# Optimization experiments

Measured on AMD Instinct MI355X. Metric: run time of the kernel, lower is better.

Reference implementation:

```python
import jax, jax.numpy as jnp
import numpy as np
from jax import lax

EPS = 1e-5
K = 7
G = 4


def _dwconv_bn(x, w, g, b, m, v):
    # depthwise 3x3, pad 1, then BN (eval mode with running stats)
    C = x.shape[1]
    y = lax.conv_general_dilated(x, w, (1, 1), [(1, 1), (1, 1)],
                                 feature_group_count=C,
                                 dimension_numbers=('NCHW', 'OIHW', 'NCHW'))
    scale = (g / jnp.sqrt(v + EPS))[None, :, None, None]
    return (y - m[None, :, None, None]) * scale + b[None, :, None, None]


def _proj(t, pw1, pb1, pw2, pb2):
    # 1x1 conv -> GELU(exact) -> 1x1 conv, on small spatial maps
    h = jnp.einsum('bchw,oc->bohw', t, pw1) + pb1[None, :, None, None]
    h = jax.nn.gelu(h, approximate=False)
    return jnp.einsum('bchw,oc->bohw', h, pw2) + pb2[None, :, None, None]


def setup_inputs() -> dict:
    key = jax.random.key(0)
    ks = jax.random.split(key, 17)
    B, C, H, W = 16, 256, 56, 56
    r = C // 4
    inp = {
        'x1': jax.random.normal(ks[0], (B, C, H, W), jnp.float32),
        'dw1_w': jax.random.normal(ks[1], (C, 1, 3, 3), jnp.float32) * 0.1,
        'dw1_g': jax.random.uniform(ks[2], (C,), jnp.float32, 0.5, 1.5),
        'dw1_b': jax.random.normal(ks[3], (C,), jnp.float32) * 0.1,
        'dw1_m': jax.random.normal(ks[4], (C,), jnp.float32) * 0.1,
        'dw1_v': jax.random.uniform(ks[5], (C,), jnp.float32, 0.5, 1.5),
        'dw2_w': jax.random.normal(ks[6], (C, 1, 3, 3), jnp.float32) * 0.1,
        'dw2_g': jax.random.uniform(ks[7], (C,), jnp.float32, 0.5, 1.5),
        'dw2_b': jax.random.normal(ks[8], (C,), jnp.float32) * 0.1,
        'dw2_m': jax.random.normal(ks[9], (C,), jnp.float32) * 0.1,
        'dw2_v': jax.random.uniform(ks[10], (C,), jnp.float32, 0.5, 1.5),
        'weight1': jax.random.normal(ks[11], (G, C, K, K), jnp.float32) * 0.02,
        'bias1': jax.random.normal(ks[12], (G, C), jnp.float32) * 0.02,
        'pw1': jax.random.normal(ks[13], (r, C), jnp.float32) * 0.05,
        'pb1': jax.random.normal(ks[14], (r,), jnp.float32) * 0.05,
        'pw2': jax.random.normal(ks[15], (C * G, r), jnp.float32) * 0.05,
        'pb2': jax.random.normal(ks[16], (C * G,), jnp.float32) * 0.05,
    }
    return inp


def reference(x1, dw1_w, dw1_g, dw1_b, dw1_m, dw1_v,
              dw2_w, dw2_g, dw2_b, dw2_m, dw2_v,
              weight1, bias1, pw1, pb1, pw2, pb2):
    B, C, H, W = x1.shape
    # gated fuse: relu6(dw1(x)) * dw2(x)
    a = jnp.clip(_dwconv_bn(x1, dw1_w, dw1_g, dw1_b, dw1_m, dw1_v), 0.0, 6.0)
    x_fuse = a * _dwconv_bn(x1, dw2_w, dw2_g, dw2_b, dw2_m, dw2_v)

    # adaptive avg pool to (K,K): H,W multiples of K -> uniform block means
    pooled = x_fuse.reshape(B, C, K, H // K, K, W // K).mean(axis=(3, 5))

    # dynamic kernel: proj -> softmax over groups -> weighted sum of weight1
    scale1 = _proj(pooled, pw1, pb1, pw2, pb2).reshape(B, G, C, K, K)
    scale1 = jax.nn.softmax(scale1, axis=1)
    w_dyn = jnp.sum(scale1 * weight1[None], axis=1)  # [B, C, K, K]

    # dynamic bias
    mean_x = x_fuse.mean(axis=(-2, -1), keepdims=True)  # [B, C, 1, 1]
    sb = _proj(mean_x, pw1, pb1, pw2, pb2).reshape(B, G, C)
    sb = jax.nn.softmax(sb, axis=1)
    b_dyn = jnp.sum(sb * bias1[None], axis=1)  # [B, C]

    # per-sample depthwise conv with dynamic weights
    pad = K // 2

    def per_sample(xi, wi):  # xi [C,H,W], wi [C,K,K]
        y = lax.conv_general_dilated(xi[None], wi[:, None], (1, 1),
                                     [(pad, pad), (pad, pad)],
                                     feature_group_count=C,
                                     dimension_numbers=('NCHW', 'OIHW', 'NCHW'))
        return y[0]

    out = jax.vmap(per_sample)(x_fuse, w_dyn)  # [B, C, H, W]
    return out + b_dyn[:, :, None, None]
```

## Files before the change

kernel.cpp:

```cpp
#include <hip/hip_runtime.h>
#include <math.h>

#define BATCH 16
#define CH 256
#define HW 56
#define NPIX (HW*HW)
#define PR 62
#define PS 64
#define PPLANE (PR*PS)

__device__ __forceinline__ void fuse_tile(
    const float* __restrict__ plane, int ty, int tx,
    const float w1[9], const float w2[9],
    float sc1, float be1, float sc2, float be2,
    float res[4][4])
{
    const int oy = 4 * ty;
    float y1a[4][4], y2a[4][4];
    #pragma unroll
    for (int a = 0; a < 4; a++)
        #pragma unroll
        for (int e = 0; e < 4; e++) { y1a[a][e] = 0.f; y2a[a][e] = 0.f; }

    #pragma unroll
    for (int iy = 0; iy < 6; iy++) {
        const int r    = oy - 1 + iy;
        const bool rok = (r >= 0) && (r < 56);
        const int rc   = rok ? r : 0;
        float rb[12];
        #pragma unroll
        for (int k = 0; k < 3; k++) {
            const int cx  = tx - 1 + k;
            const bool cv = (cx >= 0) && (cx < 14);
            const int cc2 = cv ? cx : 0;
            const bool ok = rok && cv;
            float4 v = *(const float4*)(plane + rc*56 + 4*cc2);
            rb[4*k+0] = ok ? v.x : 0.f;
            rb[4*k+1] = ok ? v.y : 0.f;
            rb[4*k+2] = ok ? v.z : 0.f;
            rb[4*k+3] = ok ? v.w : 0.f;
        }
        #pragma unroll
        for (int tyy = 0; tyy < 4; tyy++) {
            const int ky = iy - tyy;
            if (ky >= 0 && ky < 3) {
                #pragma unroll
                for (int e = 0; e < 4; e++)
                    #pragma unroll
                    for (int dj = 0; dj < 3; dj++) {
                        float xv = rb[3 + e + dj];
                        y1a[tyy][e] += xv * w1[ky*3+dj];
                        y2a[tyy][e] += xv * w2[ky*3+dj];
                    }
            }
        }
    }
    #pragma unroll
    for (int tyy = 0; tyy < 4; tyy++)
        #pragma unroll
        for (int e = 0; e < 4; e++) {
            float y1 = y1a[tyy][e] * sc1 + be1;
            float y2 = y2a[tyy][e] * sc2 + be2;
            float a = fminf(fmaxf(y1, 0.f), 6.f);
            res[tyy][e] = a * y2;
        }
}

__global__ __launch_bounds__(256) void k1_fuse(
    const float* __restrict__ x1,
    const float* __restrict__ dw1w, const float* __restrict__ g1, const float* __restrict__ b1,
    const float* __restrict__ m1, const float* __restrict__ v1,
    const float* __restrict__ dw2w, const float* __restrict__ g2, const float* __restrict__ b2,
    const float* __restrict__ m2, const float* __restrict__ v2,
    float* __restrict__ xf,
    float* __restrict__ pooled)
{
    const int bc = blockIdx.x;
    const int c  = bc & 255;
    const int t  = threadIdx.x;

    __shared__ float part[196];

    float w1[9], w2[9];
    #pragma unroll
    for (int k = 0; k < 9; k++) { w1[k] = dw1w[c*9+k]; w2[k] = dw2w[c*9+k]; }
    const float sc1 = g1[c] * rsqrtf(v1[c] + 1e-5f);
    const float be1 = b1[c] - m1[c] * sc1;
    const float sc2 = g2[c] * rsqrtf(v2[c] + 1e-5f);
    const float be2 = b2[c] - m2[c] * sc2;

    const int ty = t / 14, tx = t - ty * 14;
    float res[4][4];
    if (t < 196) {
        fuse_tile(x1 + (size_t)bc * NPIX, ty, tx, w1, w2, sc1, be1, sc2, be2, res);
        float s = 0.f;
        #pragma unroll
        for (int a = 0; a < 4; a++)
            #pragma unroll
            for (int e = 0; e < 4; e++) s += res[a][e];
        part[t] = s;
    }
    __syncthreads();

    float* xfp = xf + (size_t)bc * PPLANE;
    if (t < 49) {
        int ph = t / 7, pw = t - ph * 7;
        float s = part[(2*ph  )*14 + 2*pw] + part[(2*ph  )*14 + 2*pw + 1]
                + part[(2*ph+1)*14 + 2*pw] + part[(2*ph+1)*14 + 2*pw + 1];
        pooled[(size_t)bc * 49 + t] = s * (1.f/64.f);
    }
    if (t < 196) {
        #pragma unroll
        for (int tyy = 0; tyy < 4; tyy++) {
            float4 r4; r4.x=res[tyy][0]; r4.y=res[tyy][1]; r4.z=res[tyy][2]; r4.w=res[tyy][3];
            *(float4*)&xfp[(4*ty + tyy + 3)*PS + 4 + 4*tx] = r4;
        }
    }
    if (t < 208) {
        float4 z = make_float4(0.f, 0.f, 0.f, 0.f);
        int prow, pc4;
        if (t < 96) { int r = t >> 4; prow = (r < 3) ? r : (r + 56); pc4 = t & 15; }
        else        { int t2 = t - 96; prow = 3 + (t2 >> 1); pc4 = (t2 & 1) ? 15 : 0; }
        *(float4*)&xfp[prow*PS + 4*pc4] = z;
    }
}

__global__ __launch_bounds__(256) void k2a(
    const float* __restrict__ pooled, const float* __restrict__ pw1,
    const float* __restrict__ pb1, float* __restrict__ h)
{
    const int b  = blockIdx.x;
    const int oc = blockIdx.y;
    const int t  = threadIdx.x;
    __shared__ float pl[256*50];

    const float* pp = pooled + (size_t)b * 256 * 49;
    for (int idx = t; idx < 256*49; idx += 256) {
        int cc = idx / 49, p = idx - cc * 49;
        pl[cc*50 + p] = pp[idx];
    }
    __syncthreads();
    {
        float s = 0.f;
        #pragma unroll
        for (int p = 0; p < 49; p++) s += pl[t*50 + p];
        pl[t*50 + 49] = s * (1.f/49.f);
    }
    __syncthreads();

    for (int idx = t; idx < 16*50; idx += 256) {
        int ol = idx / 50, p = idx - ol * 50;
        int o = oc * 16 + ol;
        const float* wrow = pw1 + o * 256;
        float acc = pb1[o];
        #pragma unroll 8
        for (int cc = 0; cc < 256; cc++) acc += wrow[cc] * pl[cc*50 + p];
        float gv = 0.5f * acc * (1.f + erff(acc * 0.70710678118654752f));
        h[((size_t)b * 50 + p) * 64 + o] = gv;
    }
}

__global__ __launch_bounds__(256) void k2b(
    const float* __restrict__ h, const float* __restrict__ pw2, const float* __restrict__ pb2,
    const float* __restrict__ weight1, const float* __restrict__ bias1,
    float* __restrict__ w_dyn, float* __restrict__ b_dyn)
{
    const int b   = blockIdx.x;
    const int cch = blockIdx.y;
    const int t   = threadIdx.x;
    const int c_base = cch * 16;

    __shared__ __attribute__((aligned(16))) float hl[50*64];
    __shared__ float sl[64*51];

    const float* hp = h + (size_t)b * 50 * 64;
    for (int i = t; i < 800; i += 256) ((float4*)hl)[i] = ((const float4*)hp)[i];

    const int row = t & 63;
    const int pb  = t >> 6;
    const int g   = row >> 4, cl = row & 15;
    const int o2  = (g << 8) + c_base + cl;

    float wreg[64];
    {
        const float4* w4 = (const float4*)(pw2 + (size_t)o2 * 64);
        #pragma unroll
        for (int r4 = 0; r4 < 16; r4++) {
            float4 v = w4[r4];
            wreg[4*r4] = v.x; wreg[4*r4+1] = v.y; wreg[4*r4+2] = v.z; wreg[4*r4+3] = v.w;
        }
    }
    const float bias2 = pb2[o2];
    __syncthreads();

    for (int p = pb; p < 50; p += 4) {
        const float4* hv = (const float4*)&hl[p*64];
        float acc = bias2;
        #pragma unroll
        for (int r4 = 0; r4 < 16; r4++) {
            float4 v = hv[r4];
            acc += wreg[4*r4]*v.x + wreg[4*r4+1]*v.y + wreg[4*r4+2]*v.z + wreg[4*r4+3]*v.w;
        }
        sl[row*51 + p] = acc;
    }
    __syncthreads();

    for (int idx = t; idx < 16*50; idx += 256) {
        int cl2 = idx / 50, p = idx - cl2 * 50;
        float s0 = sl[(cl2     )*51 + p];
        float s1 = sl[(16 + cl2)*51 + p];
        float s2 = sl[(32 + cl2)*51 + p];
        float s3 = sl[(48 + cl2)*51 + p];
        float mx = fmaxf(fmaxf(s0, s1), fmaxf(s2, s3));
        float e0 = expf(s0-mx), e1 = expf(s1-mx), e2 = expf(s2-mx), e3 = expf(s3-mx);
        float inv = 1.f / (e0+e1+e2+e3);
        e0 *= inv; e1 *= inv; e2 *= inv; e3 *= inv;
        int cc = c_base + cl2;
        if (p < 49) {
            float wv = e0*weight1[(0*256+cc)*49+p] + e1*weight1[(1*256+cc)*49+p]
                     + e2*weight1[(2*256+cc)*49+p] + e3*weight1[(3*256+cc)*49+p];
            w_dyn[((size_t)b*256 + cc)*49 + p] = wv;
        } else {
            b_dyn[b*256 + cc] = e0*bias1[cc] + e1*bias1[256+cc] + e2*bias1[512+cc] + e3*bias1[768+cc];
        }
    }
}

__global__ __launch_bounds__(256) void k3_dyn(
    const float* __restrict__ xf,
    const float* __restrict__ w_dyn, const float* __restrict__ b_dyn,
    float* __restrict__ out)
{
    const int bc = blockIdx.x;
    const int t  = threadIdx.x;

    float wk[49];
    const float* wp = w_dyn + (size_t)bc * 49;
    #pragma unroll
    for (int k = 0; k < 49; k++) wk[k] = wp[k];
    const float bias = b_dyn[bc];

    if (t < 196) {
        const int ty = t / 14, tx = t - ty * 14;
        const float* xfp = xf + (size_t)bc * PPLANE + 4*tx;
        float acc[4][4];
        #pragma unroll
        for (int a = 0; a < 4; a++)
            #pragma unroll
            for (int bb = 0; bb < 4; bb++) acc[a][bb] = bias;

        #pragma unroll
        for (int iy = 0; iy < 10; iy++) {
            const float* hr = xfp + (4*ty + iy) * PS;
            float4 a = *(const float4*)hr;
            float4 b = *(const float4*)(hr + 4);
            float4 c = *(const float4*)(hr + 8);
            float row[12];
            row[0]=a.x; row[1]=a.y; row[2]=a.z; row[3]=a.w;
            row[4]=b.x; row[5]=b.y; row[6]=b.z; row[7]=b.w;
            row[8]=c.x; row[9]=c.y; row[10]=c.z; row[11]=c.w;
            #pragma unroll
            for (int tyy = 0; tyy < 4; tyy++) {
                const int ky = iy - tyy;
                if (ky >= 0 && ky < 7) {
                    #pragma unroll
                    for (int txx = 0; txx < 4; txx++)
                        #pragma unroll
                        for (int kx = 0; kx < 7; kx++)
                            acc[tyy][txx] += row[1+txx+kx] * wk[ky*7+kx];
                }
            }
        }
        float* op = out + (size_t)bc * NPIX;
        #pragma unroll
        for (int tyy = 0; tyy < 4; tyy++) {
            float4 r4; r4.x = acc[tyy][0]; r4.y = acc[tyy][1]; r4.z = acc[tyy][2]; r4.w = acc[tyy][3];
            *(float4*)(op + (4*ty+tyy)*56 + 4*tx) = r4;
        }
    }
}

extern "C" void kernel_launch(void* const* d_in, const int* in_sizes, int n_in,
                              void* d_out, int out_size, void* d_ws, size_t ws_size,
                              hipStream_t stream) {
    const float* x1    = (const float*)d_in[0];
    const float* dw1w  = (const float*)d_in[1];
    const float* dw1g  = (const float*)d_in[2];
    const float* dw1b  = (const float*)d_in[3];
    const float* dw1m  = (const float*)d_in[4];
    const float* dw1v  = (const float*)d_in[5];
    const float* dw2w  = (const float*)d_in[6];
    const float* dw2g  = (const float*)d_in[7];
    const float* dw2b  = (const float*)d_in[8];
    const float* dw2m  = (const float*)d_in[9];
    const float* dw2v  = (const float*)d_in[10];
    const float* weight1 = (const float*)d_in[11];
    const float* bias1   = (const float*)d_in[12];
    const float* pw1     = (const float*)d_in[13];
    const float* pb1     = (const float*)d_in[14];
    const float* pw2     = (const float*)d_in[15];
    const float* pb2     = (const float*)d_in[16];

    float* out = (float*)d_out;
    float* ws  = (float*)d_ws;
    float* xfuse  = ws;
    float* pooled = ws + 16252928;
    float* h      = ws + 16453632;
    float* w_dyn  = ws + 16504832;
    float* b_dyn  = ws + 16705536;

    k1_fuse<<<BATCH*CH, 256, 0, stream>>>(x1, dw1w, dw1g, dw1b, dw1m, dw1v,
                                          dw2w, dw2g, dw2b, dw2m, dw2v, xfuse, pooled);
    k2a<<<dim3(BATCH, 4), 256, 0, stream>>>(pooled, pw1, pb1, h);
    k2b<<<dim3(BATCH, 16), 256, 0, stream>>>(h, pw2, pb2, weight1, bias1, w_dyn, b_dyn);
    k3_dyn<<<BATCH*CH, 256, 0, stream>>>(xfuse, w_dyn, b_dyn, out);
}
```

Before: 207.5 us.

## Fuse projection kernels, hoist global loads ahead of weight setup, set min-blocks bounds

Merges the two small projection kernels into one. Each block now recomputes the first 1x1 conv and GELU for all 64 hidden channels in shared memory, so the intermediate buffer round trip and one launch go away. In the two large conv kernels, all input tile loads are issued into registers before the per-channel weights and BN constants are loaded, so memory latency can overlap the setup. Launch bounds request 3 blocks per SM. The trade-offs are higher register pressure from the prefetch arrays, 4x redundant first-projection work across channel chunks, and more shared memory per block in the fused projection kernel.

```diff
diff --git a/kernel.cpp b/kernel.cpp
--- a/kernel.cpp
+++ b/kernel.cpp
@@ -9,64 +9,7 @@
 #define PS 64
 #define PPLANE (PR*PS)
 
-__device__ __forceinline__ void fuse_tile(
-    const float* __restrict__ plane, int ty, int tx,
-    const float w1[9], const float w2[9],
-    float sc1, float be1, float sc2, float be2,
-    float res[4][4])
-{
-    const int oy = 4 * ty;
-    float y1a[4][4], y2a[4][4];
-    #pragma unroll
-    for (int a = 0; a < 4; a++)
-        #pragma unroll
-        for (int e = 0; e < 4; e++) { y1a[a][e] = 0.f; y2a[a][e] = 0.f; }
-
-    #pragma unroll
-    for (int iy = 0; iy < 6; iy++) {
-        const int r    = oy - 1 + iy;
-        const bool rok = (r >= 0) && (r < 56);
-        const int rc   = rok ? r : 0;
-        float rb[12];
-        #pragma unroll
-        for (int k = 0; k < 3; k++) {
-            const int cx  = tx - 1 + k;
-            const bool cv = (cx >= 0) && (cx < 14);
-            const int cc2 = cv ? cx : 0;
-            const bool ok = rok && cv;
-            float4 v = *(const float4*)(plane + rc*56 + 4*cc2);
-            rb[4*k+0] = ok ? v.x : 0.f;
-            rb[4*k+1] = ok ? v.y : 0.f;
-            rb[4*k+2] = ok ? v.z : 0.f;
-            rb[4*k+3] = ok ? v.w : 0.f;
-        }
-        #pragma unroll
-        for (int tyy = 0; tyy < 4; tyy++) {
-            const int ky = iy - tyy;
-            if (ky >= 0 && ky < 3) {
-                #pragma unroll
-                for (int e = 0; e < 4; e++)
-                    #pragma unroll
-                    for (int dj = 0; dj < 3; dj++) {
-                        float xv = rb[3 + e + dj];
-                        y1a[tyy][e] += xv * w1[ky*3+dj];
-                        y2a[tyy][e] += xv * w2[ky*3+dj];
-                    }
-            }
-        }
-    }
-    #pragma unroll
-    for (int tyy = 0; tyy < 4; tyy++)
-        #pragma unroll
-        for (int e = 0; e < 4; e++) {
-            float y1 = y1a[tyy][e] * sc1 + be1;
-            float y2 = y2a[tyy][e] * sc2 + be2;
-            float a = fminf(fmaxf(y1, 0.f), 6.f);
-            res[tyy][e] = a * y2;
-        }
-}
-
-__global__ __launch_bounds__(256) void k1_fuse(
+__global__ __launch_bounds__(256, 3) void k1_fuse(
     const float* __restrict__ x1,
     const float* __restrict__ dw1w, const float* __restrict__ g1, const float* __restrict__ b1,
     const float* __restrict__ m1, const float* __restrict__ v1,
@@ -81,6 +24,28 @@
 
     __shared__ float part[196];
 
+    const int ty = t / 14, tx = t - ty * 14;
+    const float* plane = x1 + (size_t)bc * NPIX;
+
+    float4 ld[18];
+    bool   okm[18];
+    if (t < 196) {
+        #pragma unroll
+        for (int iy = 0; iy < 6; iy++) {
+            const int r    = 4*ty - 1 + iy;
+            const bool rok = (r >= 0) && (r < 56);
+            const int rc   = rok ? r : 0;
+            #pragma unroll
+            for (int k = 0; k < 3; k++) {
+                const int cx  = tx - 1 + k;
+                const bool cv = (cx >= 0) && (cx < 14);
+                const int cc2 = cv ? cx : 0;
+                okm[iy*3+k] = rok && cv;
+                ld[iy*3+k]  = *(const float4*)(plane + rc*56 + 4*cc2);
+            }
+        }
+    }
+
     float w1[9], w2[9];
     #pragma unroll
     for (int k = 0; k < 9; k++) { w1[k] = dw1w[c*9+k]; w2[k] = dw2w[c*9+k]; }
@@ -89,15 +54,52 @@
     const float sc2 = g2[c] * rsqrtf(v2[c] + 1e-5f);
     const float be2 = b2[c] - m2[c] * sc2;
 
-    const int ty = t / 14, tx = t - ty * 14;
     float res[4][4];
     if (t < 196) {
-        fuse_tile(x1 + (size_t)bc * NPIX, ty, tx, w1, w2, sc1, be1, sc2, be2, res);
+        float y1a[4][4], y2a[4][4];
+        #pragma unroll
+        for (int a = 0; a < 4; a++)
+            #pragma unroll
+            for (int e = 0; e < 4; e++) { y1a[a][e] = 0.f; y2a[a][e] = 0.f; }
+
+        #pragma unroll
+        for (int iy = 0; iy < 6; iy++) {
+            float rb[12];
+            #pragma unroll
+            for (int k = 0; k < 3; k++) {
+                const float4 v = ld[iy*3+k];
+                const bool ok  = okm[iy*3+k];
+                rb[4*k+0] = ok ? v.x : 0.f;
+                rb[4*k+1] = ok ? v.y : 0.f;
+                rb[4*k+2] = ok ? v.z : 0.f;
+                rb[4*k+3] = ok ? v.w : 0.f;
+            }
+            #pragma unroll
+            for (int tyy = 0; tyy < 4; tyy++) {
+                const int ky = iy - tyy;
+                if (ky >= 0 && ky < 3) {
+                    #pragma unroll
+                    for (int e = 0; e < 4; e++)
+                        #pragma unroll
+                        for (int dj = 0; dj < 3; dj++) {
+                            float xv = rb[3 + e + dj];
+                            y1a[tyy][e] += xv * w1[ky*3+dj];
+                            y2a[tyy][e] += xv * w2[ky*3+dj];
+                        }
+                }
+            }
+        }
         float s = 0.f;
         #pragma unroll
-        for (int a = 0; a < 4; a++)
-            #pragma unroll
-            for (int e = 0; e < 4; e++) s += res[a][e];
+        for (int tyy = 0; tyy < 4; tyy++)
+            #pragma unroll
+            for (int e = 0; e < 4; e++) {
+                float y1 = y1a[tyy][e] * sc1 + be1;
+                float y2 = y2a[tyy][e] * sc2 + be2;
+                float a = fminf(fmaxf(y1, 0.f), 6.f);
+                res[tyy][e] = a * y2;
+                s += res[tyy][e];
+            }
         part[t] = s;
     }
     __syncthreads();
@@ -125,43 +127,10 @@
     }
 }
 
-__global__ __launch_bounds__(256) void k2a(
+__global__ __launch_bounds__(256) void k2_dyn(
     const float* __restrict__ pooled, const float* __restrict__ pw1,
-    const float* __restrict__ pb1, float* __restrict__ h)
-{
-    const int b  = blockIdx.x;
-    const int oc = blockIdx.y;
-    const int t  = threadIdx.x;
-    __shared__ float pl[256*50];
-
-    const float* pp = pooled + (size_t)b * 256 * 49;
-    for (int idx = t; idx < 256*49; idx += 256) {
-        int cc = idx / 49, p = idx - cc * 49;
-        pl[cc*50 + p] = pp[idx];
-    }
-    __syncthreads();
-    {
-        float s = 0.f;
-        #pragma unroll
-        for (int p = 0; p < 49; p++) s += pl[t*50 + p];
-        pl[t*50 + 49] = s * (1.f/49.f);
-    }
-    __syncthreads();
-
-    for (int idx = t; idx < 16*50; idx += 256) {
-        int ol = idx / 50, p = idx - ol * 50;
-        int o = oc * 16 + ol;
-        const float* wrow = pw1 + o * 256;
-        float acc = pb1[o];
-        #pragma unroll 8
-        for (int cc = 0; cc < 256; cc++) acc += wrow[cc] * pl[cc*50 + p];
-        float gv = 0.5f * acc * (1.f + erff(acc * 0.70710678118654752f));
-        h[((size_t)b * 50 + p) * 64 + o] = gv;
-    }
-}
-
-__global__ __launch_bounds__(256) void k2b(
-    const float* __restrict__ h, const float* __restrict__ pw2, const float* __restrict__ pb2,
+    const float* __restrict__ pb1, const float* __restrict__ pw2,
+    const float* __restrict__ pb2,
     const float* __restrict__ weight1, const float* __restrict__ bias1,
     float* __restrict__ w_dyn, float* __restrict__ b_dyn)
 {
@@ -170,17 +139,20 @@
     const int t   = threadIdx.x;
     const int c_base = cch * 16;
 
+    __shared__ float pl[256*50];
     __shared__ __attribute__((aligned(16))) float hl[50*64];
     __shared__ float sl[64*51];
 
-    const float* hp = h + (size_t)b * 50 * 64;
-    for (int i = t; i < 800; i += 256) ((float4*)hl)[i] = ((const float4*)hp)[i];
+    const float* pp = pooled + (size_t)b * 256 * 49;
+    for (int idx = t; idx < 256*49; idx += 256) {
+        int cc = idx / 49, p = idx - cc * 49;
+        pl[cc*50 + p] = pp[idx];
+    }
 
     const int row = t & 63;
-    const int pb  = t >> 6;
+    const int pb_ = t >> 6;
     const int g   = row >> 4, cl = row & 15;
     const int o2  = (g << 8) + c_base + cl;
-
     float wreg[64];
     {
         const float4* w4 = (const float4*)(pw2 + (size_t)o2 * 64);
@@ -193,7 +165,25 @@
     const float bias2 = pb2[o2];
     __syncthreads();
 
-    for (int p = pb; p < 50; p += 4) {
+    {
+        float s = 0.f;
+        #pragma unroll
+        for (int p = 0; p < 49; p++) s += pl[t*50 + p];
+        pl[t*50 + 49] = s * (1.f/49.f);
+    }
+    __syncthreads();
+
+    for (int idx = t; idx < 50*64; idx += 256) {
+        int p = idx >> 6, o = idx & 63;
+        const float* wrow = pw1 + o * 256;
+        float acc = pb1[o];
+        #pragma unroll 8
+        for (int cc = 0; cc < 256; cc++) acc += wrow[cc] * pl[cc*50 + p];
+        hl[idx] = 0.5f * acc * (1.f + erff(acc * 0.70710678118654752f));
+    }
+    __syncthreads();
+
+    for (int p = pb_; p < 50; p += 4) {
         const float4* hv = (const float4*)&hl[p*64];
         float acc = bias2;
         #pragma unroll
@@ -226,7 +216,7 @@
     }
 }
 
-__global__ __launch_bounds__(256) void k3_dyn(
+__global__ __launch_bounds__(256, 3) void k3_dyn(
     const float* __restrict__ xf,
     const float* __restrict__ w_dyn, const float* __restrict__ b_dyn,
     float* __restrict__ out)
@@ -234,6 +224,20 @@
     const int bc = blockIdx.x;
     const int t  = threadIdx.x;
 
+    const int ty = t / 14, tx = t - ty * 14;
+    const float* xfp = xf + (size_t)bc * PPLANE + 4*tx;
+
+    float4 ld[30];
+    if (t < 196) {
+        #pragma unroll
+        for (int iy = 0; iy < 10; iy++) {
+            const float* hr = xfp + (4*ty + iy) * PS;
+            ld[iy*3+0] = *(const float4*)hr;
+            ld[iy*3+1] = *(const float4*)(hr + 4);
+            ld[iy*3+2] = *(const float4*)(hr + 8);
+        }
+    }
+
     float wk[49];
     const float* wp = w_dyn + (size_t)bc * 49;
     #pragma unroll
@@ -241,8 +245,6 @@
     const float bias = b_dyn[bc];
 
     if (t < 196) {
-        const int ty = t / 14, tx = t - ty * 14;
-        const float* xfp = xf + (size_t)bc * PPLANE + 4*tx;
         float acc[4][4];
         #pragma unroll
         for (int a = 0; a < 4; a++)
@@ -251,10 +253,9 @@
 
         #pragma unroll
         for (int iy = 0; iy < 10; iy++) {
-            const float* hr = xfp + (4*ty + iy) * PS;
-            float4 a = *(const float4*)hr;
-            float4 b = *(const float4*)(hr + 4);
-            float4 c = *(const float4*)(hr + 8);
+            float4 a = ld[iy*3+0];
+            float4 b = ld[iy*3+1];
+            float4 c = ld[iy*3+2];
             float row[12];
             row[0]=a.x; row[1]=a.y; row[2]=a.z; row[3]=a.w;
             row[4]=b.x; row[5]=b.y; row[6]=b.z; row[7]=b.w;
@@ -305,13 +306,12 @@
     float* ws  = (float*)d_ws;
     float* xfuse  = ws;
     float* pooled = ws + 16252928;
-    float* h      = ws + 16453632;
-    float* w_dyn  = ws + 16504832;
-    float* b_dyn  = ws + 16705536;
+    float* w_dyn  = ws + 16453632;
+    float* b_dyn  = ws + 16654336;
 
     k1_fuse<<<BATCH*CH, 256, 0, stream>>>(x1, dw1w, dw1g, dw1b, dw1m, dw1v,
                                           dw2w, dw2g, dw2b, dw2m, dw2v, xfuse, pooled);
-    k2a<<<dim3(BATCH, 4), 256, 0, stream>>>(pooled, pw1, pb1, h);
-    k2b<<<dim3(BATCH, 16), 256, 0, stream>>>(h, pw2, pb2, weight1, bias1, w_dyn, b_dyn);
+    k2_dyn<<<dim3(BATCH, 16), 256, 0, stream>>>(pooled, pw1, pb1, pw2, pb2,
+                                                weight1, bias1, w_dyn, b_dyn);
     k3_dyn<<<BATCH*CH, 256, 0, stream>>>(xfuse, w_dyn, b_dyn, out);
 }
```

New measurement: 275.0 us. 1.33x slower.
